# Kernel tuning notes

Hardware: AMD Instinct MI355X
Metric: run time of the kernel (lower is better)

## Reference

```python
import jax, jax.numpy as jnp
import numpy as np

BINS = 256
VMIN = 0.0
VMAX = 1.0
SIGMA = 30.0
DELTA = (VMAX - VMIN) / BINS


def setup_inputs() -> dict:
    key = jax.random.key(0)
    y = jax.random.uniform(key, (4, 1, 512, 512), dtype=jnp.float32)
    return {"y": y}


def reference(y) -> jnp.ndarray:
    b, _, h, w = y.shape
    yf = y.reshape(b, 1, -1)                      # (b, 1, h*w)
    centers = VMIN + DELTA * (jnp.arange(BINS, dtype=jnp.float32) + 0.5)
    c = centers.reshape(1, BINS, 1)               # (1, bins, 1)
    x = yf - c                                    # (b, bins, h*w) broadcast
    k = jax.nn.sigmoid(SIGMA * (x + DELTA / 2)) - jax.nn.sigmoid(SIGMA * (x - DELTA / 2))
    hist = jnp.sum(k, axis=2)                     # (b, bins)
    p = hist / (h * w) + 1e-6
    d = jnp.sum(-p * jnp.log(p))
    return 1.0 / d
```

## Files before the change

kernel.cpp:

```cpp
#include <hip/hip_runtime.h>
#include <math.h>

#define NB 4
#define BINS 256
#define HW (512*512)

#define CHUNKS 64
#define PIX_PER_BLOCK (HW / CHUNKS)
#define F4_PER_THREAD (PIX_PER_BLOCK / 4 / 256)

#define MCH 8
#define MPB (BINS / MCH)


__global__ __launch_bounds__(256) void hist_moments(const float* __restrict__ y,
                                                    float* __restrict__ Hg,
                                                    float* __restrict__ Sg) {
    __shared__ float lh[BINS];
    __shared__ float ls[BINS];
    const int t = threadIdx.x;
    lh[t] = 0.0f;
    ls[t] = 0.0f;
    __syncthreads();

    const int b = blockIdx.y;
    const float4* src = reinterpret_cast<const float4*>(
        y + (size_t)b * HW + (size_t)blockIdx.x * PIX_PER_BLOCK);

#pragma unroll
    for (int i = 0; i < F4_PER_THREAD; ++i) {
        float4 v = src[t + 256 * i];
        float vals[4] = {v.x, v.y, v.z, v.w};
#pragma unroll
        for (int c = 0; c < 4; ++c) {
            float f = vals[c];
            int bin = (int)(f * 256.0f);
            bin = bin < 0 ? 0 : (bin > 255 ? 255 : bin);
            atomicAdd(&lh[bin], 1.0f);
            atomicAdd(&ls[bin], f);
        }
    }
    __syncthreads();
    atomicAdd(&Hg[b * BINS + t], lh[t]);
    atomicAdd(&Sg[b * BINS + t], ls[t]);
}

__global__ __launch_bounds__(256) void conv_kernel(const float* __restrict__ Hg,
                                                   const float* __restrict__ Sg,
                                                   float* __restrict__ Pg) {
    __shared__ float2 K01[2 * BINS];
    __shared__ float2 HM[MPB];

    const int t = threadIdx.x;
    const int b = blockIdx.y;
    const int m0 = blockIdx.x * MPB;
    const float DELTA = 1.0f / 256.0f;
    const float SIGMA = 30.0f;

    for (int i = t; i < 2 * BINS - 1; i += 256) {
        float x = (float)(i - (BINS - 1)) * DELTA;
        float zp = SIGMA * (x + 0.5f * DELTA);
        float zm = SIGMA * (x - 0.5f * DELTA);
        float sp = 1.0f / (1.0f + __expf(-zp));
        float sm = 1.0f / (1.0f + __expf(-zm));
        K01[i] = make_float2(sp - sm,
                             SIGMA * (sp * (1.0f - sp) - sm * (1.0f - sm)));
    }
    if (t < MPB) {
        int m = m0 + t;
        float H  = Hg[b * BINS + m];
        float M1 = Sg[b * BINS + m] - H * ((float)m + 0.5f) * DELTA;
        HM[t] = make_float2(H, M1);
    }
    __syncthreads();

    const int j = t;
    float acc = 0.0f;
#pragma unroll 8
    for (int mm = 0; mm < MPB; ++mm) {
        float2 hm = HM[mm];
        float2 k  = K01[m0 + mm - j + (BINS - 1)];
        acc = fmaf(hm.x, k.x, acc);
        acc = fmaf(hm.y, k.y, acc);
    }
    atomicAdd(&Pg[b * BINS + j], acc);
}

__global__ __launch_bounds__(1024) void entropy_kernel(const float* __restrict__ Pg,
                                                       float* __restrict__ out) {
    __shared__ float red[16];
    const int t = threadIdx.x;
    float p = Pg[t] * (1.0f / (float)HW) + 1e-6f;
    float e = -p * __logf(p);
    const int lane = t & 63, wid = t >> 6;
#pragma unroll
    for (int off = 32; off > 0; off >>= 1) e += __shfl_down(e, off);
    if (lane == 0) red[wid] = e;
    __syncthreads();
    if (t == 0) {
        float d = 0.0f;
#pragma unroll
        for (int i = 0; i < 16; ++i) d += red[i];
        out[0] = 1.0f / d;
    }
}

extern "C" void kernel_launch(void* const* d_in, const int* in_sizes, int n_in,
                              void* d_out, int out_size, void* d_ws, size_t ws_size,
                              hipStream_t stream) {
    const float* y = (const float*)d_in[0];
    float* Hg = (float*)d_ws;
    float* Sg = Hg + NB * BINS;
    float* Pg = Sg + NB * BINS;

    hipMemsetAsync(d_ws, 0, 3 * NB * BINS * sizeof(float), stream);
    hist_moments<<<dim3(CHUNKS, NB), 256, 0, stream>>>(y, Hg, Sg);
    conv_kernel<<<dim3(MCH, NB), 256, 0, stream>>>(Hg, Sg, Pg);
    entropy_kernel<<<1, 1024, 0, stream>>>(Pg, (float*)d_out);
}
```

Baseline: 70.34 us.

## Fuse conv and entropy into one kernel, drop memset and global atomics

The histogram kernel now writes per-chunk partial histograms to workspace instead of atomically adding into global bins. The convolution and entropy steps merge into one kernel with one block per batch that reduces the partials, convolves, and combines the entropy through an atomic counter with last-block finalisation. This removes the memset launch and one kernel launch, cutting launch overhead and global atomic contention. In exchange it adds a serial partial reduction and leaves only 4 blocks in the second kernel, so little parallelism is available there.

```diff
diff --git a/kernel.cpp b/kernel.cpp
--- a/kernel.cpp
+++ b/kernel.cpp
@@ -9,18 +9,20 @@
 #define PIX_PER_BLOCK (HW / CHUNKS)
 #define F4_PER_THREAD (PIX_PER_BLOCK / 4 / 256)
 
-#define MCH 8
-#define MPB (BINS / MCH)
 
-
-__global__ __launch_bounds__(256) void hist_moments(const float* __restrict__ y,
-                                                    float* __restrict__ Hg,
-                                                    float* __restrict__ Sg) {
+__global__ __launch_bounds__(256) void hist_part(const float* __restrict__ y,
+                                                 float* __restrict__ Hp,
+                                                 float* __restrict__ Sp,
+                                                 float* __restrict__ acc) {
     __shared__ float lh[BINS];
     __shared__ float ls[BINS];
     const int t = threadIdx.x;
     lh[t] = 0.0f;
     ls[t] = 0.0f;
+    if (blockIdx.x == 0 && blockIdx.y == 0 && t == 0) {
+        acc[0] = 0.0f;
+        ((unsigned*)acc)[1] = 0u;
+    }
     __syncthreads();
 
     const int b = blockIdx.y;
@@ -41,21 +43,33 @@
         }
     }
     __syncthreads();
-    atomicAdd(&Hg[b * BINS + t], lh[t]);
-    atomicAdd(&Sg[b * BINS + t], ls[t]);
+    const size_t o = ((size_t)b * CHUNKS + blockIdx.x) * BINS + t;
+    Hp[o] = lh[t];
+    Sp[o] = ls[t];
 }
 
-__global__ __launch_bounds__(256) void conv_kernel(const float* __restrict__ Hg,
-                                                   const float* __restrict__ Sg,
-                                                   float* __restrict__ Pg) {
-    __shared__ float2 K01[2 * BINS];
-    __shared__ float2 HM[MPB];
+__global__ __launch_bounds__(256) void entropy_fused(const float* __restrict__ Hp,
+                                                     const float* __restrict__ Sp,
+                                                     float* __restrict__ acc,
+                                                     float* __restrict__ out) {
+    __shared__ float2 K01[512];
+    __shared__ float2 HM[BINS];
+    __shared__ float red[4];
 
     const int t = threadIdx.x;
-    const int b = blockIdx.y;
-    const int m0 = blockIdx.x * MPB;
+    const int b = blockIdx.x;
     const float DELTA = 1.0f / 256.0f;
     const float SIGMA = 30.0f;
+
+    float H = 0.0f, S = 0.0f;
+    const float* hb = Hp + (size_t)b * CHUNKS * BINS + t;
+    const float* sb = Sp + (size_t)b * CHUNKS * BINS + t;
+#pragma unroll 8
+    for (int c = 0; c < CHUNKS; ++c) {
+        H += hb[c * BINS];
+        S += sb[c * BINS];
+    }
+    HM[t] = make_float2(H, S - H * ((float)t + 0.5f) * DELTA);
 
     for (int i = t; i < 2 * BINS - 1; i += 256) {
         float x = (float)(i - (BINS - 1)) * DELTA;
@@ -66,42 +80,37 @@
         K01[i] = make_float2(sp - sm,
                              SIGMA * (sp * (1.0f - sp) - sm * (1.0f - sm)));
     }
-    if (t < MPB) {
-        int m = m0 + t;
-        float H  = Hg[b * BINS + m];
-        float M1 = Sg[b * BINS + m] - H * ((float)m + 0.5f) * DELTA;
-        HM[t] = make_float2(H, M1);
-    }
     __syncthreads();
 
     const int j = t;
-    float acc = 0.0f;
+    float hist = 0.0f;
 #pragma unroll 8
-    for (int mm = 0; mm < MPB; ++mm) {
-        float2 hm = HM[mm];
-        float2 k  = K01[m0 + mm - j + (BINS - 1)];
-        acc = fmaf(hm.x, k.x, acc);
-        acc = fmaf(hm.y, k.y, acc);
+    for (int m = 0; m < BINS; ++m) {
+        float2 hm = HM[m];
+        float2 k  = K01[m - j + (BINS - 1)];
+        hist = fmaf(hm.x, k.x, hist);
+        hist = fmaf(hm.y, k.y, hist);
     }
-    atomicAdd(&Pg[b * BINS + j], acc);
-}
 
-__global__ __launch_bounds__(1024) void entropy_kernel(const float* __restrict__ Pg,
-                                                       float* __restrict__ out) {
-    __shared__ float red[16];
-    const int t = threadIdx.x;
-    float p = Pg[t] * (1.0f / (float)HW) + 1e-6f;
+    float p = hist * (1.0f / (float)HW) + 1e-6f;
     float e = -p * __logf(p);
+
     const int lane = t & 63, wid = t >> 6;
 #pragma unroll
     for (int off = 32; off > 0; off >>= 1) e += __shfl_down(e, off);
     if (lane == 0) red[wid] = e;
     __syncthreads();
+
     if (t == 0) {
-        float d = 0.0f;
-#pragma unroll
-        for (int i = 0; i < 16; ++i) d += red[i];
-        out[0] = 1.0f / d;
+        float part = red[0] + red[1] + red[2] + red[3];
+        atomicAdd(acc, part);
+        __threadfence();
+        unsigned old = atomicAdd(((unsigned*)acc) + 1, 1u);
+        if (old == NB - 1) {
+            __threadfence();
+            float d = atomicAdd(acc, 0.0f);
+            out[0] = 1.0f / d;
+        }
     }
 }
 
@@ -109,12 +118,10 @@
                               void* d_out, int out_size, void* d_ws, size_t ws_size,
                               hipStream_t stream) {
     const float* y = (const float*)d_in[0];
-    float* Hg = (float*)d_ws;
-    float* Sg = Hg + NB * BINS;
-    float* Pg = Sg + NB * BINS;
+    float* Hp = (float*)d_ws;
+    float* Sp = Hp + NB * CHUNKS * BINS;
+    float* acc = Sp + NB * CHUNKS * BINS;
 
-    hipMemsetAsync(d_ws, 0, 3 * NB * BINS * sizeof(float), stream);
-    hist_moments<<<dim3(CHUNKS, NB), 256, 0, stream>>>(y, Hg, Sg);
-    conv_kernel<<<dim3(MCH, NB), 256, 0, stream>>>(Hg, Sg, Pg);
-    entropy_kernel<<<1, 1024, 0, stream>>>(Pg, (float*)d_out);
+    hist_part<<<dim3(CHUNKS, NB), 256, 0, stream>>>(y, Hp, Sp, acc);
+    entropy_fused<<<NB, 256, 0, stream>>>(Hp, Sp, acc, (float*)d_out);
 }
```

Measured after the change: 71.36 us. About the same (+1.4%).
